# Performance work log

Hardware: AMD Instinct MI355X
Metric: run time of the kernel (lower is better)

## Reference

```python
import jax, jax.numpy as jnp
import numpy as np

CUTOFF = 5.0
N_RBF = 20
N_NODES = 16384
N_EDGES = 262144
HID = 128


def setup_inputs() -> dict:
    key = jax.random.key(0)
    ks = jax.random.split(key, 8)
    s = jax.random.normal(ks[0], (N_NODES, HID), dtype=jnp.float32)
    v = jax.random.normal(ks[1], (N_NODES, 3, HID), dtype=jnp.float32)
    r_ij = jax.random.normal(ks[2], (N_EDGES, 3), dtype=jnp.float32)
    edge_src = jax.random.randint(ks[3], (N_EDGES,), 0, N_NODES, dtype=jnp.int32)
    edge_dst = jax.random.randint(ks[4], (N_EDGES,), 0, N_NODES, dtype=jnp.int32)
    W1 = jax.random.normal(ks[5], (HID, HID), dtype=jnp.float32) / np.sqrt(HID)
    b1 = jnp.zeros((HID,), dtype=jnp.float32)
    W2 = jax.random.normal(ks[6], (HID, 3 * HID), dtype=jnp.float32) / np.sqrt(HID)
    b2 = jnp.zeros((3 * HID,), dtype=jnp.float32)
    Wrbf = jax.random.normal(ks[7], (N_RBF, 3 * HID), dtype=jnp.float32) / np.sqrt(N_RBF)
    brbf = jnp.zeros((3 * HID,), dtype=jnp.float32)
    return {"s": s, "v": v, "r_ij": r_ij, "edge_src": edge_src, "edge_dst": edge_dst,
            "W1": W1, "b1": b1, "W2": W2, "b2": b2, "Wrbf": Wrbf, "brbf": brbf}


def reference(s, v, r_ij, edge_src, edge_dst, W1, b1, W2, b2, Wrbf, brbf):
    n_nodes = s.shape[0]
    # distances & unit directions
    d = jnp.linalg.norm(r_ij, axis=-1, keepdims=True)            # [E,1]
    unit = r_ij / d                                              # [E,3]
    # sinc radial basis: sin(n*pi*d/cutoff)/d, n = 1..N_RBF
    n = jnp.arange(1, N_RBF + 1, dtype=s.dtype)
    rbf = jnp.sin(n * jnp.pi * d / CUTOFF) / d                   # [E,20]
    # cosine cutoff
    fcut = 0.5 * (jnp.cos(jnp.pi * d / CUTOFF) + 1.0) * (d < CUTOFF)  # [E,1]
    # scalar filter phi(s): Linear -> SiLU -> Linear, then gather to edges
    phi = jax.nn.silu(s @ W1 + b1) @ W2 + b2                     # [N,384]
    phi_j = phi[edge_src]                                        # [E,384]
    # radial filter, cutoff-weighted
    W = (rbf @ Wrbf + brbf) * fcut                               # [E,384]
    split = phi_j * W                                            # [E,384] hadamard
    x_vv = split[:, :HID]          # gates gathered v_j
    x_s = split[:, HID:2 * HID]    # scalar message
    x_dir = split[:, 2 * HID:]     # gates direction vectors
    # per-edge vector message: v_j * x_vv + unit ⊗ x_dir
    dv_edge = v[edge_src] * x_vv[:, None, :] + unit[:, :, None] * x_dir[:, None, :]  # [E,3,128]
    # scatter-sum to destination nodes
    ds = jax.ops.segment_sum(x_s, edge_dst, num_segments=n_nodes)       # [N,128]
    dv = jax.ops.segment_sum(dv_edge, edge_dst, num_segments=n_nodes)   # [N,3,128]
    return dv, ds
```

## Files before the change

kernel.cpp:

```cpp
#include <hip/hip_runtime.h>
#include <math.h>
#include <stdint.h>

#define N_NODES 16384
#define N_EDGES 262144
#define HID 128
#define NRBF 20
#define CUTOFF 5.0f
#define PI_F 3.14159265358979323846f

#define CSTRIDE 16

typedef __attribute__((ext_vector_type(2))) __fp16 half2_t;
union U32H2 { uint32_t u; half2_t h; float f; };

__device__ inline unsigned short f2bf(float f) {
    unsigned int u = __float_as_uint(f);
    u = u + 0x7FFFu + ((u >> 16) & 1u);
    return (unsigned short)(u >> 16);
}
__device__ inline uint32_t pack2(float lo, float hi) {
    return (uint32_t)f2bf(lo) | ((uint32_t)f2bf(hi) << 16);
}
__device__ inline float blo(uint32_t u) { return __uint_as_float(u << 16); }
__device__ inline float bhi(uint32_t u) { return __uint_as_float(u & 0xFFFF0000u); }
__device__ inline uint32_t pkh2(float a, float b) {
    U32H2 u; u.h = __builtin_amdgcn_cvt_pkrtz(a, b); return u.u;
}

__global__ __launch_bounds__(256) void prep_kernel(
    const float* __restrict__ W1, const float* __restrict__ W2,
    const float* __restrict__ Wrbf, const int* __restrict__ edst,
    int* __restrict__ cnt, uint32_t* __restrict__ W1p,
    uint32_t* __restrict__ W2p, uint32_t* __restrict__ Wrbfp)
{
    const int id = blockIdx.x * 256 + threadIdx.x;
    if (id < 8192) {
        const int kp = id >> 7, t = id & 127;
        W1p[id] = pkh2(W1[(size_t)(2 * kp) * HID + t],
                       W1[(size_t)(2 * kp + 1) * HID + t]);
    } else if (id < 32768) {
        const int i = id - 8192;
        const int kp = i / 384, rem = i % 384;
        W2p[i] = pkh2(W2[(size_t)(2 * kp) * 384 + rem],
                      W2[(size_t)(2 * kp + 1) * 384 + rem]);
    } else if (id < 36608) {
        const int i = id - 32768;
        const int j = i / 384, rem = i % 384;
        Wrbfp[i] = pkh2(Wrbf[(size_t)(2 * j) * 384 + rem],
                        Wrbf[(size_t)(2 * j + 1) * 384 + rem]);
    } else if (id < 36608 + N_EDGES) {
        atomicAdd(&cnt[edst[id - 36608]], 1);
    }
}

__global__ __launch_bounds__(256) void scan_kernel(const int* __restrict__ cnt,
                                                   int* __restrict__ row_ptr,
                                                   int* __restrict__ cur)
{
    __shared__ int part[256];
    const int tid = threadIdx.x;
    const int4* c4 = (const int4*)cnt;

    int4 loc[16];
    int s = 0;
    #pragma unroll
    for (int j = 0; j < 16; ++j) {
        loc[j] = c4[tid * 16 + j];
        s += loc[j].x + loc[j].y + loc[j].z + loc[j].w;
    }
    part[tid] = s;
    __syncthreads();
    #pragma unroll
    for (int d = 1; d < 256; d <<= 1) {
        const int add = (tid >= d) ? part[tid - d] : 0;
        __syncthreads();
        part[tid] += add;
        __syncthreads();
    }
    int off = (tid == 0) ? 0 : part[tid - 1];
    const int base = tid * 64;
    #pragma unroll
    for (int j = 0; j < 16; ++j) {
        const int4 q = loc[j];
        row_ptr[base + j*4 + 0] = off; cur[base + j*4 + 0] = off; off += q.x;
        row_ptr[base + j*4 + 1] = off; cur[base + j*4 + 1] = off; off += q.y;
        row_ptr[base + j*4 + 2] = off; cur[base + j*4 + 2] = off; off += q.z;
        row_ptr[base + j*4 + 3] = off; cur[base + j*4 + 3] = off; off += q.w;
    }
    if (tid == 255) row_ptr[16384] = off;
}

#define PB 32
__global__ __launch_bounds__(512, 4) void phi_scatter_kernel(
    const float* __restrict__ s, const float* __restrict__ v,
    const uint32_t* __restrict__ W1p, const float* __restrict__ b1,
    const uint32_t* __restrict__ W2p, const float* __restrict__ b2,
    const float* __restrict__ r_ij, const int* __restrict__ esrc,
    const int* __restrict__ edst, int* __restrict__ cur,
    int* __restrict__ soff, uint32_t* __restrict__ coef,
    uint2* __restrict__ guv, uint32_t* __restrict__ gw)
{
    const int tid = threadIdx.x;
    const int ch  = tid & 127;
    const int sub = tid >> 7;
    const int node0 = blockIdx.x * PB;

    {
        const int e = blockIdx.x * 512 + tid;
        const float rx = r_ij[(size_t)e * 3 + 0];
        const float ry = r_ij[(size_t)e * 3 + 1];
        const float rz = r_ij[(size_t)e * 3 + 2];
        const float d = sqrtf(rx * rx + ry * ry + rz * rz);
        const float inv_d = 1.0f / d;
        float sx, cx;
        sincosf((PI_F / CUTOFF) * d, &sx, &cx);
        const float fcut = (d < CUTOFF) ? 0.5f * (cx + 1.0f) : 0.0f;

        float cf[NRBF];
        const float gfac = inv_d * fcut;
        const float twocx = 2.0f * cx;
        float sm1 = sx, sm2 = 0.0f;
        cf[0] = sx * gfac;
        #pragma unroll
        for (int n = 1; n < NRBF; ++n) {
            const float sn = twocx * sm1 - sm2;
            sm2 = sm1; sm1 = sn;
            cf[n] = sn * gfac;
        }

        uint32_t cp[10];
        #pragma unroll
        for (int j = 0; j < 10; ++j) cp[j] = pkh2(cf[2 * j], cf[2 * j + 1]);

        const int pos = atomicAdd(&cur[edst[e]], 1);
        soff[pos] = esrc[e] * 128;
        uint4* c4 = (uint4*)(coef + (size_t)pos * CSTRIDE);
        c4[0] = make_uint4(__float_as_uint(rx * inv_d),
                           __float_as_uint(ry * inv_d),
                           __float_as_uint(rz * inv_d),
                           __float_as_uint(fcut));
        c4[1] = make_uint4(cp[0], cp[1], cp[2], cp[3]);
        c4[2] = make_uint4(cp[4], cp[5], cp[6], cp[7]);
        c4[3] = make_uint4(cp[8], cp[9], 0u, 0u);
    }

    __shared__ uint32_t sL2[PB][64];
    __shared__ float    hL[PB][HID];
    __shared__ uint32_t hL2[PB][64];

    #pragma unroll
    for (int q = 0; q < 4; ++q) {
        const int idx = q * 512 + tid;
        const int i = idx >> 6, c = idx & 63;
        const float2 sv = *(const float2*)&s[(size_t)(node0 + i) * HID + 2 * c];
        sL2[i][c] = pkh2(sv.x, sv.y);
    }
    __syncthreads();

    float h[8];
    const float bb1 = b1[ch];
    #pragma unroll
    for (int i = 0; i < 8; ++i) h[i] = bb1;

    for (int kp = 0; kp < 64; kp += 2) {
        U32H2 wa; wa.u = W1p[kp * 128 + ch];
        U32H2 wb; wb.u = W1p[(kp + 1) * 128 + ch];
        #pragma unroll
        for (int i = 0; i < 8; ++i) {
            U32H2 ca; ca.u = sL2[sub * 8 + i][kp];
            U32H2 cb; cb.u = sL2[sub * 8 + i][kp + 1];
            h[i] = __builtin_amdgcn_fdot2(ca.h, wa.h, h[i], false);
            h[i] = __builtin_amdgcn_fdot2(cb.h, wb.h, h[i], false);
        }
    }
    #pragma unroll
    for (int i = 0; i < 8; ++i) {
        const float x = h[i];
        hL[sub * 8 + i][ch] = x / (1.0f + expf(-x));
    }
    __syncthreads();
    #pragma unroll
    for (int q = 0; q < 4; ++q) {
        const int idx = q * 512 + tid;
        const int i = idx >> 6, c = idx & 63;
        hL2[i][c] = pkh2(hL[i][2 * c], hL[i][2 * c + 1]);
    }
    __syncthreads();

    float a0[8], a1[8], a2[8];
    #pragma unroll
    for (int i = 0; i < 8; ++i) { a0[i] = 0.f; a1[i] = 0.f; a2[i] = 0.f; }

    for (int kp = 0; kp < 64; ++kp) {
        U32H2 wA; wA.u = W2p[(kp * 3 + 0) * 128 + ch];
        U32H2 wB; wB.u = W2p[(kp * 3 + 1) * 128 + ch];
        U32H2 wC; wC.u = W2p[(kp * 3 + 2) * 128 + ch];
        #pragma unroll
        for (int i = 0; i < 8; ++i) {
            U32H2 hh; hh.u = hL2[sub * 8 + i][kp];
            a0[i] = __builtin_amdgcn_fdot2(hh.h, wA.h, a0[i], false);
            a1[i] = __builtin_amdgcn_fdot2(hh.h, wB.h, a1[i], false);
            a2[i] = __builtin_amdgcn_fdot2(hh.h, wC.h, a2[i], false);
        }
    }
    const float bb2a = b2[ch], bb2b = b2[128 + ch], bb2c = b2[256 + ch];
    #pragma unroll
    for (int i = 0; i < 8; ++i) {
        const int node = node0 + sub * 8 + i;
        const size_t nrow = (size_t)node * 384;
        const float p0 = a0[i] + bb2a;
        const float p1 = a1[i] + bb2b;
        const float p2 = a2[i] + bb2c;
        const float v0 = v[nrow + ch];
        const float v1 = v[nrow + 128 + ch];
        const float v2 = v[nrow + 256 + ch];
        const size_t gi = (size_t)node * HID + ch;
        guv[gi] = make_uint2(pack2(p0, p1), pack2(p2, v0));
        gw[gi]  = pack2(v1, v2);
    }
}

__global__ __launch_bounds__(256, 6) void gather_kernel(
    const uint2* __restrict__ guv, const uint32_t* __restrict__ gw,
    const int* __restrict__ soff, const uint32_t* __restrict__ coef,
    const int* __restrict__ row_ptr, const uint32_t* __restrict__ Wrbfp,
    const float* __restrict__ brbf,
    float* __restrict__ dv, float* __restrict__ ds)
{
    const int ch   = threadIdx.x & 127;
    const int node = blockIdx.x * 2 + (threadIdx.x >> 7);

    uint32_t wq0[10], wq1[10], wq2[10];
    #pragma unroll
    for (int j = 0; j < 10; ++j) {
        wq0[j] = Wrbfp[(j * 3 + 0) * 128 + ch];
        wq1[j] = Wrbfp[(j * 3 + 1) * 128 + ch];
        wq2[j] = Wrbfp[(j * 3 + 2) * 128 + ch];
    }
    #pragma unroll
    for (int j = 0; j < 10; ++j) {
        asm volatile("" : "+v"(wq0[j]), "+v"(wq1[j]), "+v"(wq2[j]));
    }
    const float br0 = brbf[ch], br1 = brbf[128 + ch], br2 = brbf[256 + ch];

    const int beg = row_ptr[node];
    const int end = row_ptr[node + 1];
    const int nb  = (end - beg) >> 2;

    float a0 = 0.f, a1 = 0.f, a2 = 0.f, as = 0.f;

    uint2 A2[4], B2[4];
    uint32_t Aw[4], Bw[4];

#define LOADB(P2, Pw, bi) do {                                                \
    const int iu_ = __builtin_amdgcn_readfirstlane(beg + (bi) * 4);           \
    const int* sp_ = soff + iu_;                                              \
    const int o0 = sp_[0] + ch, o1 = sp_[1] + ch,                             \
              o2 = sp_[2] + ch, o3 = sp_[3] + ch;                             \
    P2[0] = guv[o0]; P2[1] = guv[o1]; P2[2] = guv[o2]; P2[3] = guv[o3];       \
    Pw[0] = gw[o0];  Pw[1] = gw[o1];  Pw[2] = gw[o2];  Pw[3] = gw[o3];        \
    const uint32_t* cq_ = coef + (size_t)iu_ * CSTRIDE;                       \
    const uint32_t t0_ = cq_[0],  t1_ = cq_[16],                              \
                   t2_ = cq_[32], t3_ = cq_[48];                              \
    asm volatile("" :: "s"(t0_), "s"(t1_), "s"(t2_), "s"(t3_));               \
} while (0)

#define CONSUME(P2, Pw, bi) do {                                              \
    const uint32_t* cp_ = coef +                                              \
        (size_t)__builtin_amdgcn_readfirstlane(beg + (bi) * 4) * CSTRIDE;     \
    _Pragma("unroll")                                                         \
    for (int k = 0; k < 4; ++k) {                                             \
        const float ux = __uint_as_float(cp_[k * CSTRIDE + 0]);               \
        const float uy = __uint_as_float(cp_[k * CSTRIDE + 1]);               \
        const float uz = __uint_as_float(cp_[k * CSTRIDE + 2]);               \
        const float fc = __uint_as_float(cp_[k * CSTRIDE + 3]);               \
        float W0 = fc * br0;                                                  \
        float W1 = fc * br1;                                                  \
        float W2 = fc * br2;                                                  \
        _Pragma("unroll")                                                     \
        for (int j = 0; j < 10; ++j) {                                        \
            U32H2 cc; cc.u = cp_[k * CSTRIDE + 4 + j];                        \
            U32H2 w0_; w0_.u = wq0[j];                                        \
            U32H2 w1_; w1_.u = wq1[j];                                        \
            U32H2 w2_; w2_.u = wq2[j];                                        \
            W0 = __builtin_amdgcn_fdot2(cc.h, w0_.h, W0, false);              \
            W1 = __builtin_amdgcn_fdot2(cc.h, w1_.h, W1, false);              \
            W2 = __builtin_amdgcn_fdot2(cc.h, w2_.h, W2, false);              \
        }                                                                     \
        const uint32_t p0 = P2[k].x, p1 = P2[k].y, p2 = Pw[k];                \
        const float xv = blo(p0) * W0;                                        \
        const float xs = bhi(p0) * W1;                                        \
        const float xd = blo(p1) * W2;                                        \
        a0 += bhi(p1) * xv + ux * xd;                                         \
        a1 += blo(p2) * xv + uy * xd;                                         \
        a2 += bhi(p2) * xv + uz * xd;                                         \
        as += xs;                                                             \
    }                                                                         \
} while (0)

    if (nb > 0) {
        const int last = nb - 1;
        LOADB(A2, Aw, 0);
        LOADB(B2, Bw, (1 < last ? 1 : last));
        int b = 0;
        for (; b + 2 < nb; b += 2) {
            CONSUME(A2, Aw, b);
            LOADB(A2, Aw, b + 2);
            CONSUME(B2, Bw, b + 1);
            LOADB(B2, Bw, (b + 3 < last ? b + 3 : last));
        }
        const int rem = nb - b;
        CONSUME(A2, Aw, b);
        if (rem == 2) CONSUME(B2, Bw, b + 1);
    }

    for (int i = beg + (nb << 2); i < end; ++i) {
        const int iu = __builtin_amdgcn_readfirstlane(i);
        const int o = soff[iu] + ch;
        const uint2 P = guv[o];
        const uint32_t p2 = gw[o];
        const uint32_t* cp = coef + (size_t)iu * CSTRIDE;
        const float ux = __uint_as_float(cp[0]);
        const float uy = __uint_as_float(cp[1]);
        const float uz = __uint_as_float(cp[2]);
        const float fc = __uint_as_float(cp[3]);
        float W0 = fc * br0;
        float W1 = fc * br1;
        float W2 = fc * br2;
        #pragma unroll
        for (int j = 0; j < 10; ++j) {
            U32H2 cc; cc.u = cp[4 + j];
            U32H2 w0_; w0_.u = wq0[j];
            U32H2 w1_; w1_.u = wq1[j];
            U32H2 w2_; w2_.u = wq2[j];
            W0 = __builtin_amdgcn_fdot2(cc.h, w0_.h, W0, false);
            W1 = __builtin_amdgcn_fdot2(cc.h, w1_.h, W1, false);
            W2 = __builtin_amdgcn_fdot2(cc.h, w2_.h, W2, false);
        }
        const uint32_t p0 = P.x, p1 = P.y;
        const float xv = blo(p0) * W0;
        const float xs = bhi(p0) * W1;
        const float xd = blo(p1) * W2;
        a0 += bhi(p1) * xv + ux * xd;
        a1 += blo(p2) * xv + uy * xd;
        a2 += bhi(p2) * xv + uz * xd;
        as += xs;
    }

#undef LOADB
#undef CONSUME

    const size_t orow = (size_t)node * 384;
    dv[orow + ch]       = a0;
    dv[orow + 128 + ch] = a1;
    dv[orow + 256 + ch] = a2;
    ds[(size_t)node * HID + ch] = as;
}

extern "C" void kernel_launch(void* const* d_in, const int* in_sizes, int n_in,
                              void* d_out, int out_size, void* d_ws, size_t ws_size,
                              hipStream_t stream)
{
    const float* s    = (const float*)d_in[0];
    const float* v    = (const float*)d_in[1];
    const float* r_ij = (const float*)d_in[2];
    const int*   esrc = (const int*)d_in[3];
    const int*   edst = (const int*)d_in[4];
    const float* W1   = (const float*)d_in[5];
    const float* b1   = (const float*)d_in[6];
    const float* W2   = (const float*)d_in[7];
    const float* b2   = (const float*)d_in[8];
    const float* Wrbf = (const float*)d_in[9];
    const float* brbf = (const float*)d_in[10];

    float* out = (float*)d_out;
    float* dv  = out;
    float* ds  = out + (size_t)N_NODES * 3 * HID;

    char* ws = (char*)d_ws;
    uint2*    guv     = (uint2*)   (ws + 0);
    uint32_t* gw      = (uint32_t*)(ws + 16777216);
    uint32_t* coef    = (uint32_t*)(ws + 25165824);
    int*      soff    = (int*)     (ws + 41943040);
    int*      cnt     = (int*)     (ws + 42991616);
    int*      row_ptr = (int*)     (ws + 43057152);
    int*      cur     = (int*)     (ws + 43122816);
    uint32_t* W1p     = (uint32_t*)(ws + 43188352);
    uint32_t* W2p     = (uint32_t*)(ws + 43221120);
    uint32_t* Wrbfp   = (uint32_t*)(ws + 43319424);

    hipMemsetAsync(cnt, 0, 16384 * sizeof(int), stream);

    prep_kernel<<<1167, 256, 0, stream>>>(W1, W2, Wrbf, edst, cnt,
                                          W1p, W2p, Wrbfp);
    scan_kernel<<<1, 256, 0, stream>>>(cnt, row_ptr, cur);
    phi_scatter_kernel<<<512, 512, 0, stream>>>(s, v, W1p, b1, W2p, b2,
                                                r_ij, esrc, edst, cur,
                                                soff, coef, guv, gw);
    gather_kernel<<<N_NODES / 2, 256, 0, stream>>>(guv, gw, soff, coef, row_ptr,
                                                   Wrbfp, brbf, dv, ds);
}
```

Before: 136.6 us.

## Compute node MLP with MFMA 16x16x16 fp16 using fragment-packed weights

```diff
diff --git a/kernel.cpp b/kernel.cpp
--- a/kernel.cpp
+++ b/kernel.cpp
@@ -12,7 +12,10 @@
 #define CSTRIDE 16
 
 typedef __attribute__((ext_vector_type(2))) __fp16 half2_t;
+typedef __attribute__((ext_vector_type(4))) __fp16 v4h;
+typedef __attribute__((ext_vector_type(4))) float f32x4;
 union U32H2 { uint32_t u; half2_t h; float f; };
+union U2H4 { uint32_t u[2]; v4h h; };
 
 __device__ inline unsigned short f2bf(float f) {
     unsigned int u = __float_as_uint(f);
@@ -31,19 +34,23 @@
 __global__ __launch_bounds__(256) void prep_kernel(
     const float* __restrict__ W1, const float* __restrict__ W2,
     const float* __restrict__ Wrbf, const int* __restrict__ edst,
-    int* __restrict__ cnt, uint32_t* __restrict__ W1p,
-    uint32_t* __restrict__ W2p, uint32_t* __restrict__ Wrbfp)
+    int* __restrict__ cnt, uint32_t* __restrict__ W1f,
+    uint32_t* __restrict__ W2f, uint32_t* __restrict__ Wrbfp)
 {
     const int id = blockIdx.x * 256 + threadIdx.x;
     if (id < 8192) {
-        const int kp = id >> 7, t = id & 127;
-        W1p[id] = pkh2(W1[(size_t)(2 * kp) * HID + t],
-                       W1[(size_t)(2 * kp + 1) * HID + t]);
+        const int c = id >> 10, rem = id & 1023;
+        const int ks = rem >> 7, l = (rem & 127) >> 1, p = rem & 1;
+        const int k = ks * 16 + 4 * (l >> 4) + 2 * p;
+        const int col = c * 16 + (l & 15);
+        W1f[id] = pkh2(W1[(size_t)k * 128 + col], W1[(size_t)(k + 1) * 128 + col]);
     } else if (id < 32768) {
         const int i = id - 8192;
-        const int kp = i / 384, rem = i % 384;
-        W2p[i] = pkh2(W2[(size_t)(2 * kp) * 384 + rem],
-                      W2[(size_t)(2 * kp + 1) * 384 + rem]);
+        const int c = i >> 10, rem = i & 1023;
+        const int ks = rem >> 7, l = (rem & 127) >> 1, p = rem & 1;
+        const int k = ks * 16 + 4 * (l >> 4) + 2 * p;
+        const int col = c * 16 + (l & 15);
+        W2f[i] = pkh2(W2[(size_t)k * 384 + col], W2[(size_t)(k + 1) * 384 + col]);
     } else if (id < 36608) {
         const int i = id - 32768;
         const int j = i / 384, rem = i % 384;
@@ -91,23 +98,26 @@
     if (tid == 255) row_ptr[16384] = off;
 }
 
-#define PB 32
-__global__ __launch_bounds__(512, 4) void phi_scatter_kernel(
+#define MB 64
+__global__ __launch_bounds__(256) void phi_scatter_kernel(
     const float* __restrict__ s, const float* __restrict__ v,
-    const uint32_t* __restrict__ W1p, const float* __restrict__ b1,
-    const uint32_t* __restrict__ W2p, const float* __restrict__ b2,
+    const uint32_t* __restrict__ W1f, const float* __restrict__ b1,
+    const uint32_t* __restrict__ W2f, const float* __restrict__ b2,
     const float* __restrict__ r_ij, const int* __restrict__ esrc,
     const int* __restrict__ edst, int* __restrict__ cur,
     int* __restrict__ soff, uint32_t* __restrict__ coef,
     uint2* __restrict__ guv, uint32_t* __restrict__ gw)
 {
     const int tid = threadIdx.x;
-    const int ch  = tid & 127;
-    const int sub = tid >> 7;
-    const int node0 = blockIdx.x * PB;
-
-    {
-        const int e = blockIdx.x * 512 + tid;
+    const int l  = tid & 63;
+    const int w  = tid >> 6;
+    const int r  = l & 15;
+    const int g4 = l >> 4;
+    const int node0 = blockIdx.x * MB;
+
+    #pragma unroll
+    for (int q = 0; q < 4; ++q) {
+        const int e = blockIdx.x * 1024 + q * 256 + tid;
         const float rx = r_ij[(size_t)e * 3 + 0];
         const float ry = r_ij[(size_t)e * 3 + 1];
         const float rz = r_ij[(size_t)e * 3 + 2];
@@ -145,79 +155,81 @@
         c4[3] = make_uint4(cp[8], cp[9], 0u, 0u);
     }
 
-    __shared__ uint32_t sL2[PB][64];
-    __shared__ float    hL[PB][HID];
-    __shared__ uint32_t hL2[PB][64];
-
-    #pragma unroll
-    for (int q = 0; q < 4; ++q) {
-        const int idx = q * 512 + tid;
-        const int i = idx >> 6, c = idx & 63;
-        const float2 sv = *(const float2*)&s[(size_t)(node0 + i) * HID + 2 * c];
-        sL2[i][c] = pkh2(sv.x, sv.y);
-    }
-    __syncthreads();
-
-    float h[8];
-    const float bb1 = b1[ch];
-    #pragma unroll
-    for (int i = 0; i < 8; ++i) h[i] = bb1;
-
-    for (int kp = 0; kp < 64; kp += 2) {
-        U32H2 wa; wa.u = W1p[kp * 128 + ch];
-        U32H2 wb; wb.u = W1p[(kp + 1) * 128 + ch];
-        #pragma unroll
-        for (int i = 0; i < 8; ++i) {
-            U32H2 ca; ca.u = sL2[sub * 8 + i][kp];
-            U32H2 cb; cb.u = sL2[sub * 8 + i][kp + 1];
-            h[i] = __builtin_amdgcn_fdot2(ca.h, wa.h, h[i], false);
-            h[i] = __builtin_amdgcn_fdot2(cb.h, wb.h, h[i], false);
-        }
-    }
-    #pragma unroll
-    for (int i = 0; i < 8; ++i) {
-        const float x = h[i];
-        hL[sub * 8 + i][ch] = x / (1.0f + expf(-x));
-    }
-    __syncthreads();
-    #pragma unroll
-    for (int q = 0; q < 4; ++q) {
-        const int idx = q * 512 + tid;
-        const int i = idx >> 6, c = idx & 63;
-        hL2[i][c] = pkh2(hL[i][2 * c], hL[i][2 * c + 1]);
-    }
-    __syncthreads();
-
-    float a0[8], a1[8], a2[8];
-    #pragma unroll
-    for (int i = 0; i < 8; ++i) { a0[i] = 0.f; a1[i] = 0.f; a2[i] = 0.f; }
-
-    for (int kp = 0; kp < 64; ++kp) {
-        U32H2 wA; wA.u = W2p[(kp * 3 + 0) * 128 + ch];
-        U32H2 wB; wB.u = W2p[(kp * 3 + 1) * 128 + ch];
-        U32H2 wC; wC.u = W2p[(kp * 3 + 2) * 128 + ch];
-        #pragma unroll
-        for (int i = 0; i < 8; ++i) {
-            U32H2 hh; hh.u = hL2[sub * 8 + i][kp];
-            a0[i] = __builtin_amdgcn_fdot2(hh.h, wA.h, a0[i], false);
-            a1[i] = __builtin_amdgcn_fdot2(hh.h, wB.h, a1[i], false);
-            a2[i] = __builtin_amdgcn_fdot2(hh.h, wC.h, a2[i], false);
-        }
-    }
-    const float bb2a = b2[ch], bb2b = b2[128 + ch], bb2c = b2[256 + ch];
-    #pragma unroll
-    for (int i = 0; i < 8; ++i) {
-        const int node = node0 + sub * 8 + i;
-        const size_t nrow = (size_t)node * 384;
-        const float p0 = a0[i] + bb2a;
-        const float p1 = a1[i] + bb2b;
-        const float p2 = a2[i] + bb2c;
-        const float v0 = v[nrow + ch];
-        const float v1 = v[nrow + 128 + ch];
-        const float v2 = v[nrow + 256 + ch];
-        const size_t gi = (size_t)node * HID + ch;
-        guv[gi] = make_uint2(pack2(p0, p1), pack2(p2, v0));
-        gw[gi]  = pack2(v1, v2);
+    __shared__ float hL[MB][132];
+
+    f32x4 acc1[8];
+    #pragma unroll
+    for (int c = 0; c < 8; ++c) acc1[c] = (f32x4){0.f, 0.f, 0.f, 0.f};
+
+    #pragma unroll
+    for (int ks = 0; ks < 8; ++ks) {
+        const float4 sv = *(const float4*)
+            &s[(size_t)(node0 + w * 16 + r) * HID + ks * 16 + 4 * g4];
+        U2H4 af; af.u[0] = pkh2(sv.x, sv.y); af.u[1] = pkh2(sv.z, sv.w);
+        #pragma unroll
+        for (int c = 0; c < 8; ++c) {
+            const uint2 bw = *(const uint2*)&W1f[((c * 8 + ks) * 64 + l) * 2];
+            U2H4 bf; bf.u[0] = bw.x; bf.u[1] = bw.y;
+            acc1[c] = __builtin_amdgcn_mfma_f32_16x16x16f16(af.h, bf.h,
+                                                            acc1[c], 0, 0, 0);
+        }
+    }
+
+    #pragma unroll
+    for (int c = 0; c < 8; ++c) {
+        const float bb = b1[c * 16 + r];
+        #pragma unroll
+        for (int j = 0; j < 4; ++j) {
+            const float x = acc1[c][j] + bb;
+            hL[w * 16 + 4 * g4 + j][c * 16 + r] = x / (1.0f + expf(-x));
+        }
+    }
+
+    uint32_t a2f[16];
+    #pragma unroll
+    for (int ks = 0; ks < 8; ++ks) {
+        const float4 hv = *(const float4*)
+            &hL[w * 16 + r][ks * 16 + 4 * g4];
+        a2f[2 * ks]     = pkh2(hv.x, hv.y);
+        a2f[2 * ks + 1] = pkh2(hv.z, hv.w);
+    }
+
+    #pragma unroll
+    for (int c = 0; c < 8; ++c) {
+        f32x4 pA = (f32x4){0.f, 0.f, 0.f, 0.f};
+        f32x4 pB = (f32x4){0.f, 0.f, 0.f, 0.f};
+        f32x4 pC = (f32x4){0.f, 0.f, 0.f, 0.f};
+        #pragma unroll
+        for (int ks = 0; ks < 8; ++ks) {
+            U2H4 af; af.u[0] = a2f[2 * ks]; af.u[1] = a2f[2 * ks + 1];
+            const uint2 b0w = *(const uint2*)&W2f[(((c     ) * 8 + ks) * 64 + l) * 2];
+            const uint2 b1w = *(const uint2*)&W2f[(((c +  8) * 8 + ks) * 64 + l) * 2];
+            const uint2 b2w = *(const uint2*)&W2f[(((c + 16) * 8 + ks) * 64 + l) * 2];
+            U2H4 bf0; bf0.u[0] = b0w.x; bf0.u[1] = b0w.y;
+            U2H4 bf1; bf1.u[0] = b1w.x; bf1.u[1] = b1w.y;
+            U2H4 bf2; bf2.u[0] = b2w.x; bf2.u[1] = b2w.y;
+            pA = __builtin_amdgcn_mfma_f32_16x16x16f16(af.h, bf0.h, pA, 0, 0, 0);
+            pB = __builtin_amdgcn_mfma_f32_16x16x16f16(af.h, bf1.h, pB, 0, 0, 0);
+            pC = __builtin_amdgcn_mfma_f32_16x16x16f16(af.h, bf2.h, pC, 0, 0, 0);
+        }
+        const int ch = c * 16 + r;
+        const float bbA = b2[ch];
+        const float bbB = b2[128 + ch];
+        const float bbC = b2[256 + ch];
+        #pragma unroll
+        for (int j = 0; j < 4; ++j) {
+            const int node = node0 + w * 16 + 4 * g4 + j;
+            const size_t nrow = (size_t)node * 384;
+            const float p0 = pA[j] + bbA;
+            const float p1 = pB[j] + bbB;
+            const float p2 = pC[j] + bbC;
+            const float v0 = v[nrow + ch];
+            const float v1 = v[nrow + 128 + ch];
+            const float v2 = v[nrow + 256 + ch];
+            const size_t gi = (size_t)node * HID + ch;
+            guv[gi] = make_uint2(pack2(p0, p1), pack2(p2, v0));
+            gw[gi]  = pack2(v1, v2);
+        }
     }
 }
 
@@ -386,16 +398,16 @@
     int*      cnt     = (int*)     (ws + 42991616);
     int*      row_ptr = (int*)     (ws + 43057152);
     int*      cur     = (int*)     (ws + 43122816);
-    uint32_t* W1p     = (uint32_t*)(ws + 43188352);
-    uint32_t* W2p     = (uint32_t*)(ws + 43221120);
+    uint32_t* W1f     = (uint32_t*)(ws + 43188352);
+    uint32_t* W2f     = (uint32_t*)(ws + 43221120);
     uint32_t* Wrbfp   = (uint32_t*)(ws + 43319424);
 
     hipMemsetAsync(cnt, 0, 16384 * sizeof(int), stream);
 
     prep_kernel<<<1167, 256, 0, stream>>>(W1, W2, Wrbf, edst, cnt,
-                                          W1p, W2p, Wrbfp);
+                                          W1f, W2f, Wrbfp);
     scan_kernel<<<1, 256, 0, stream>>>(cnt, row_ptr, cur);
-    phi_scatter_kernel<<<512, 512, 0, stream>>>(s, v, W1p, b1, W2p, b2,
+    phi_scatter_kernel<<<256, 256, 0, stream>>>(s, v, W1f, b1, W2f, b2,
                                                 r_ij, esrc, edst, cur,
                                                 soff, coef, guv, gw);
     gather_kernel<<<N_NODES / 2, 256, 0, stream>>>(guv, gw, soff, coef, row_ptr,
```

Result: slower. 159.1 us (+16.5%).
